# Performance work log

Hardware: AMD Instinct MI355X
Metric: run time of the kernel (lower is better)

Reference implementation:

```python
import jax, jax.numpy as jnp
import numpy as np

TEMPERATURE = 2.0
N, C = 16384, 1000


def _margin(x, targets):
    """Per-row: top1 - top2 if the target class attains the max, else 0."""
    top2 = jax.lax.top_k(x, 2)[0]                                  # [N, 2]
    tval = jnp.take_along_axis(x, targets[:, None], axis=1)[:, 0]  # [N]
    return jnp.where(tval == top2[:, 0], top2[:, 0] - top2[:, 1], jnp.zeros((), x.dtype))


def setup_inputs() -> dict:
    key = jax.random.key(0)
    ks = jax.random.split(key, 8)
    outs = {f"outputs{i+1}": jax.random.normal(ks[i], (N, C), dtype=jnp.float32) for i in range(6)}
    outs["mimic"] = jax.random.normal(ks[6], (N, C), dtype=jnp.float32)
    outs["targets"] = jax.random.randint(ks[7], (N,), 0, C)
    outs["n_test"] = N
    return outs


def reference(outputs1, outputs2, outputs3, outputs4, outputs5, outputs6, mimic, targets, n_test):
    t = targets[:n_test]
    heads = [outputs1, outputs2, outputs3, outputs4, outputs5, outputs6, mimic]
    # [n_test, 7] stacked margins (d1..d6, m) in original ordering
    margins = jnp.stack([_margin(h[:n_test], t) for h in heads], axis=1)
    out_threshold = jax.nn.softmax(margins / TEMPERATURE, axis=1)
    max_preds = jnp.max(jnp.stack([outputs1, outputs2, outputs3, outputs4, outputs5, outputs6]))
    return max_preds, out_threshold
```

## Files before the change

### kernel.cpp

```cpp
#include <hip/hip_runtime.h>
#include <math.h>


#define WAVES_PER_BLOCK 4
#define ROWS_PER_WAVE 2
#define ROWS_PER_BLOCK (WAVES_PER_BLOCK * ROWS_PER_WAVE)

__global__ __launch_bounds__(256) void margin_kernel(
    const float* __restrict__ h0, const float* __restrict__ h1,
    const float* __restrict__ h2, const float* __restrict__ h3,
    const float* __restrict__ h4, const float* __restrict__ h5,
    const float* __restrict__ h6,
    const int* __restrict__ targets,
    float* __restrict__ margins,
    float* __restrict__ partials,
    int N, int C)
{
    const int lane = threadIdx.x & 63;
    const int waveInBlock = threadIdx.x >> 6;
    const int head = blockIdx.y;

    const float* base;
    switch (head) {
        case 0: base = h0; break;
        case 1: base = h1; break;
        case 2: base = h2; break;
        case 3: base = h3; break;
        case 4: base = h4; break;
        case 5: base = h5; break;
        default: base = h6; break;
    }

    const int row0 = (blockIdx.x * WAVES_PER_BLOCK + waveInBlock) * ROWS_PER_WAVE;
    const int row1 = row0 + 1;
    const float* b0 = base + (size_t)row0 * C;
    const float* b1 = base + (size_t)row1 * C;
    const float4* v0 = (const float4*)b0;
    const float4* v1 = (const float4*)b1;
    const int nvec = C >> 2;

    float4 a0 = v0[lane];
    float4 a1 = v0[64 + lane];
    float4 a2 = v0[128 + lane];
    float4 c0 = v1[lane];
    float4 c1 = v1[64 + lane];
    float4 c2 = v1[128 + lane];
    float4 a3 = make_float4(-INFINITY, -INFINITY, -INFINITY, -INFINITY);
    float4 c3 = a3;
    if (192 + lane < nvec) {
        a3 = v0[192 + lane];
        c3 = v1[192 + lane];
    }

    float m1a = -INFINITY, m2a = -INFINITY;
    float m1c = -INFINITY, m2c = -INFINITY;
    float va[16] = {a0.x,a0.y,a0.z,a0.w, a1.x,a1.y,a1.z,a1.w,
                    a2.x,a2.y,a2.z,a2.w, a3.x,a3.y,a3.z,a3.w};
    float vc[16] = {c0.x,c0.y,c0.z,c0.w, c1.x,c1.y,c1.z,c1.w,
                    c2.x,c2.y,c2.z,c2.w, c3.x,c3.y,c3.z,c3.w};
    #pragma unroll
    for (int k = 0; k < 16; ++k) {
        float x = va[k];
        m2a = fmaxf(m2a, fminf(m1a, x));
        m1a = fmaxf(m1a, x);
        float y = vc[k];
        m2c = fmaxf(m2c, fminf(m1c, y));
        m1c = fmaxf(m1c, y);
    }

    #pragma unroll
    for (int off = 32; off >= 1; off >>= 1) {
        float o1a = __shfl_xor(m1a, off);
        float o2a = __shfl_xor(m2a, off);
        float o1c = __shfl_xor(m1c, off);
        float o2c = __shfl_xor(m2c, off);
        m2a = fmaxf(fmaxf(m2a, o2a), fminf(m1a, o1a));
        m1a = fmaxf(m1a, o1a);
        m2c = fmaxf(fmaxf(m2c, o2c), fminf(m1c, o1c));
        m1c = fmaxf(m1c, o1c);
    }

    __shared__ float smax[WAVES_PER_BLOCK];
    if (lane == 0) {
        int t0 = targets[row0];
        int t1 = targets[row1];
        float tv0 = b0[t0];
        float tv1 = b1[t1];
        margins[head * N + row0] = (tv0 == m1a) ? (m1a - m2a) : 0.0f;
        margins[head * N + row1] = (tv1 == m1c) ? (m1c - m2c) : 0.0f;
        smax[waveInBlock] = fmaxf(m1a, m1c);
    }
    __syncthreads();
    if (threadIdx.x == 0 && head < 6) {
        float bm = fmaxf(fmaxf(smax[0], smax[1]), fmaxf(smax[2], smax[3]));
        partials[head * gridDim.x + blockIdx.x] = bm;
    }
}

__global__ __launch_bounds__(256) void epilogue_kernel(
    const float* __restrict__ margins, const float* __restrict__ partials,
    int npart, float* __restrict__ out, int N)
{
    if (blockIdx.x == 0) {
        float m = -INFINITY;
        for (int i = threadIdx.x; i < npart; i += 256) m = fmaxf(m, partials[i]);
        #pragma unroll
        for (int off = 32; off >= 1; off >>= 1) m = fmaxf(m, __shfl_xor(m, off));
        __shared__ float s[4];
        int lane = threadIdx.x & 63, w = threadIdx.x >> 6;
        if (lane == 0) s[w] = m;
        __syncthreads();
        if (threadIdx.x == 0)
            out[0] = fmaxf(fmaxf(s[0], s[1]), fmaxf(s[2], s[3]));
        return;
    }
    int row = (blockIdx.x - 1) * 256 + threadIdx.x;
    if (row >= N) return;
    float m[7];
    float mx = -INFINITY;
    #pragma unroll
    for (int j = 0; j < 7; ++j) { m[j] = margins[j * N + row]; mx = fmaxf(mx, m[j]); }
    float s = 0.0f;
    #pragma unroll
    for (int j = 0; j < 7; ++j) { m[j] = expf((m[j] - mx) * 0.5f); s += m[j]; }
    float inv = 1.0f / s;
    float* o = out + 1 + (size_t)row * 7;
    #pragma unroll
    for (int j = 0; j < 7; ++j) o[j] = m[j] * inv;
}

extern "C" void kernel_launch(void* const* d_in, const int* in_sizes, int n_in,
                              void* d_out, int out_size, void* d_ws, size_t ws_size,
                              hipStream_t stream) {
    const float* h0 = (const float*)d_in[0];
    const float* h1 = (const float*)d_in[1];
    const float* h2 = (const float*)d_in[2];
    const float* h3 = (const float*)d_in[3];
    const float* h4 = (const float*)d_in[4];
    const float* h5 = (const float*)d_in[5];
    const float* h6 = (const float*)d_in[6];
    const int* targets = (const int*)d_in[7];

    const int N = in_sizes[7];
    const int C = in_sizes[0] / N;

    float* margins  = (float*)d_ws;
    float* partials = margins + 7 * N;

    const int blocksX = N / ROWS_PER_BLOCK;
    const int npart = 6 * blocksX;

    dim3 grid(blocksX, 7, 1);
    margin_kernel<<<grid, 256, 0, stream>>>(h0, h1, h2, h3, h4, h5, h6,
                                            targets, margins, partials, N, C);
    epilogue_kernel<<<1 + (N + 255) / 256, 256, 0, stream>>>(margins, partials,
                                                             npart, (float*)d_out, N);
}
```

Before: 390.7 us.

## Make each wave loop over all heads with double-buffered row prefetch

Replaces the per-(rows, head) grid with a 1D grid where each wave processes four rows across all seven heads, prefetching the next task's row data and target values while reducing the current one. Target-value gathers are issued alongside the bulk loads instead of after the reduction, and the block-level shared-memory max is replaced by per-wave partials. This aims to hide memory latency and cut launch and block overhead, at the cost of higher register pressure and fewer resident waves.

```diff
diff --git a/kernel.cpp b/kernel.cpp
--- a/kernel.cpp
+++ b/kernel.cpp
@@ -3,10 +3,63 @@
 
 
 #define WAVES_PER_BLOCK 4
-#define ROWS_PER_WAVE 2
-#define ROWS_PER_BLOCK (WAVES_PER_BLOCK * ROWS_PER_WAVE)
 
-__global__ __launch_bounds__(256) void margin_kernel(
+struct Task {
+    float4 a0, a1, a2, a3;
+    float4 c0, c1, c2, c3;
+    float tv0, tv1;
+};
+
+__device__ __forceinline__ void issue_task(Task& t, const float* __restrict__ base,
+                                           int r, int C, int lane, int t0, int t1) {
+    const float* b0 = base + (size_t)r * C;
+    const float* b1 = b0 + C;
+    const float4* v0 = (const float4*)b0;
+    const float4* v1 = (const float4*)b1;
+    const int nvec = C >> 2;
+    t.a0 = v0[lane];       t.c0 = v1[lane];
+    t.a1 = v0[64 + lane];  t.c1 = v1[64 + lane];
+    t.a2 = v0[128 + lane]; t.c2 = v1[128 + lane];
+    if (192 + lane < nvec) { t.a3 = v0[192 + lane]; t.c3 = v1[192 + lane]; }
+    else {
+        t.a3 = make_float4(-INFINITY, -INFINITY, -INFINITY, -INFINITY);
+        t.c3 = t.a3;
+    }
+    t.tv0 = b0[t0];
+    t.tv1 = b1[t1];
+}
+
+__device__ __forceinline__ void reduce_task(const Task& t,
+                                            float& m1a, float& m2a,
+                                            float& m1c, float& m2c) {
+    float va[16] = {t.a0.x,t.a0.y,t.a0.z,t.a0.w, t.a1.x,t.a1.y,t.a1.z,t.a1.w,
+                    t.a2.x,t.a2.y,t.a2.z,t.a2.w, t.a3.x,t.a3.y,t.a3.z,t.a3.w};
+    float vc[16] = {t.c0.x,t.c0.y,t.c0.z,t.c0.w, t.c1.x,t.c1.y,t.c1.z,t.c1.w,
+                    t.c2.x,t.c2.y,t.c2.z,t.c2.w, t.c3.x,t.c3.y,t.c3.z,t.c3.w};
+    m1a = -INFINITY; m2a = -INFINITY; m1c = -INFINITY; m2c = -INFINITY;
+    #pragma unroll
+    for (int k = 0; k < 16; ++k) {
+        float x = va[k];
+        m2a = fmaxf(m2a, fminf(m1a, x));
+        m1a = fmaxf(m1a, x);
+        float y = vc[k];
+        m2c = fmaxf(m2c, fminf(m1c, y));
+        m1c = fmaxf(m1c, y);
+    }
+    #pragma unroll
+    for (int off = 32; off >= 1; off >>= 1) {
+        float o1a = __shfl_xor(m1a, off);
+        float o2a = __shfl_xor(m2a, off);
+        float o1c = __shfl_xor(m1c, off);
+        float o2c = __shfl_xor(m2c, off);
+        m2a = fmaxf(fmaxf(m2a, o2a), fminf(m1a, o1a));
+        m1a = fmaxf(m1a, o1a);
+        m2c = fmaxf(fmaxf(m2c, o2c), fminf(m1c, o1c));
+        m1c = fmaxf(m1c, o1c);
+    }
+}
+
+__global__ __launch_bounds__(256, 4) void margin_kernel(
     const float* __restrict__ h0, const float* __restrict__ h1,
     const float* __restrict__ h2, const float* __restrict__ h3,
     const float* __restrict__ h4, const float* __restrict__ h5,
@@ -18,83 +71,42 @@
 {
     const int lane = threadIdx.x & 63;
     const int waveInBlock = threadIdx.x >> 6;
-    const int head = blockIdx.y;
+    const int w = blockIdx.x * WAVES_PER_BLOCK + waveInBlock;
+    const int NW = N >> 2;
 
-    const float* base;
-    switch (head) {
-        case 0: base = h0; break;
-        case 1: base = h1; break;
-        case 2: base = h2; break;
-        case 3: base = h3; break;
-        case 4: base = h4; break;
-        case 5: base = h5; break;
-        default: base = h6; break;
-    }
+    const float* const hp[7] = {h0, h1, h2, h3, h4, h5, h6};
 
-    const int row0 = (blockIdx.x * WAVES_PER_BLOCK + waveInBlock) * ROWS_PER_WAVE;
-    const int row1 = row0 + 1;
-    const float* b0 = base + (size_t)row0 * C;
-    const float* b1 = base + (size_t)row1 * C;
-    const float4* v0 = (const float4*)b0;
-    const float4* v1 = (const float4*)b1;
-    const int nvec = C >> 2;
+    const int rA = 2 * w;
+    const int rB = 2 * w + (N >> 1);
+    const int tA0 = targets[rA],     tA1 = targets[rA + 1];
+    const int tB0 = targets[rB],     tB1 = targets[rB + 1];
 
-    float4 a0 = v0[lane];
-    float4 a1 = v0[64 + lane];
-    float4 a2 = v0[128 + lane];
-    float4 c0 = v1[lane];
-    float4 c1 = v1[64 + lane];
-    float4 c2 = v1[128 + lane];
-    float4 a3 = make_float4(-INFINITY, -INFINITY, -INFINITY, -INFINITY);
-    float4 c3 = a3;
-    if (192 + lane < nvec) {
-        a3 = v0[192 + lane];
-        c3 = v1[192 + lane];
-    }
+    Task cur, nxt;
+    issue_task(cur, hp[0], rA, C, lane, tA0, tA1);
 
-    float m1a = -INFINITY, m2a = -INFINITY;
-    float m1c = -INFINITY, m2c = -INFINITY;
-    float va[16] = {a0.x,a0.y,a0.z,a0.w, a1.x,a1.y,a1.z,a1.w,
-                    a2.x,a2.y,a2.z,a2.w, a3.x,a3.y,a3.z,a3.w};
-    float vc[16] = {c0.x,c0.y,c0.z,c0.w, c1.x,c1.y,c1.z,c1.w,
-                    c2.x,c2.y,c2.z,c2.w, c3.x,c3.y,c3.z,c3.w};
-    #pragma unroll
-    for (int k = 0; k < 16; ++k) {
-        float x = va[k];
-        m2a = fmaxf(m2a, fminf(m1a, x));
-        m1a = fmaxf(m1a, x);
-        float y = vc[k];
-        m2c = fmaxf(m2c, fminf(m1c, y));
-        m1c = fmaxf(m1c, y);
-    }
+    float wmax = -INFINITY;
+    float m1a, m2a, m1c, m2c;
 
     #pragma unroll
-    for (int off = 32; off >= 1; off >>= 1) {
-        float o1a = __shfl_xor(m1a, off);
-        float o2a = __shfl_xor(m2a, off);
-        float o1c = __shfl_xor(m1c, off);
-        float o2c = __shfl_xor(m2c, off);
-        m2a = fmaxf(fmaxf(m2a, o2a), fminf(m1a, o1a));
-        m1a = fmaxf(m1a, o1a);
-        m2c = fmaxf(fmaxf(m2c, o2c), fminf(m1c, o1c));
-        m1c = fmaxf(m1c, o1c);
+    for (int it = 0; it < 14; ++it) {
+        const int h = it >> 1;
+        const int s = it & 1;
+        if (it < 13) {
+            const int itn = it + 1;
+            const int hn = itn >> 1, sn = itn & 1;
+            issue_task(nxt, hp[hn], sn ? rB : rA, C, lane,
+                       sn ? tB0 : tA0, sn ? tB1 : tA1);
+        }
+        reduce_task(cur, m1a, m2a, m1c, m2c);
+        const int r = s ? rB : rA;
+        if (lane == 0) {
+            margins[h * N + r]     = (cur.tv0 == m1a) ? (m1a - m2a) : 0.0f;
+            margins[h * N + r + 1] = (cur.tv1 == m1c) ? (m1c - m2c) : 0.0f;
+        }
+        if (h < 6) wmax = fmaxf(wmax, fmaxf(m1a, m1c));
+        cur = nxt;
     }
-
-    __shared__ float smax[WAVES_PER_BLOCK];
-    if (lane == 0) {
-        int t0 = targets[row0];
-        int t1 = targets[row1];
-        float tv0 = b0[t0];
-        float tv1 = b1[t1];
-        margins[head * N + row0] = (tv0 == m1a) ? (m1a - m2a) : 0.0f;
-        margins[head * N + row1] = (tv1 == m1c) ? (m1c - m2c) : 0.0f;
-        smax[waveInBlock] = fmaxf(m1a, m1c);
-    }
-    __syncthreads();
-    if (threadIdx.x == 0 && head < 6) {
-        float bm = fmaxf(fmaxf(smax[0], smax[1]), fmaxf(smax[2], smax[3]));
-        partials[head * gridDim.x + blockIdx.x] = bm;
-    }
+    if (lane == 0) partials[w] = wmax;
 }
 
 __global__ __launch_bounds__(256) void epilogue_kernel(
@@ -107,8 +119,8 @@
         #pragma unroll
         for (int off = 32; off >= 1; off >>= 1) m = fmaxf(m, __shfl_xor(m, off));
         __shared__ float s[4];
-        int lane = threadIdx.x & 63, w = threadIdx.x >> 6;
-        if (lane == 0) s[w] = m;
+        int lane = threadIdx.x & 63, wv = threadIdx.x >> 6;
+        if (lane == 0) s[wv] = m;
         __syncthreads();
         if (threadIdx.x == 0)
             out[0] = fmaxf(fmaxf(s[0], s[1]), fmaxf(s[2], s[3]));
@@ -147,12 +159,11 @@
     float* margins  = (float*)d_ws;
     float* partials = margins + 7 * N;
 
-    const int blocksX = N / ROWS_PER_BLOCK;
-    const int npart = 6 * blocksX;
+    const int NW = N / 4;
+    const int nblocks = NW / WAVES_PER_BLOCK;
 
-    dim3 grid(blocksX, 7, 1);
-    margin_kernel<<<grid, 256, 0, stream>>>(h0, h1, h2, h3, h4, h5, h6,
-                                            targets, margins, partials, N, C);
+    margin_kernel<<<nblocks, 256, 0, stream>>>(h0, h1, h2, h3, h4, h5, h6,
+                                               targets, margins, partials, N, C);
     epilogue_kernel<<<1 + (N + 255) / 256, 256, 0, stream>>>(margins, partials,
-                                                             npart, (float*)d_out, N);
+                                                             NW, (float*)d_out, N);
 }
```

New measurement: 667.1 us. +70.7%, slower.
